# Kernel optimization log

Hardware: AMD Instinct MI355X
Metric: run time of the kernel (lower is better)

Reference implementation:

```python
import jax, jax.numpy as jnp
import numpy as np

HEADS = 8
IN_C = 256
MDL = 512
N = 4
L = 4096
NE = 65536  # avg degree 16


def setup_inputs() -> dict:
    key = jax.random.key(0)
    ks = jax.random.split(key, 14)
    f32 = jnp.float32
    s = 0.05
    return {
        "queries": jax.random.normal(ks[0], (N, L, IN_C), f32),
        "keys": jax.random.normal(ks[1], (N, L, IN_C), f32),
        "values": jax.random.normal(ks[2], (N, L, IN_C), f32),
        "adj": jax.random.randint(ks[3], (2, NE), 0, L, dtype=jnp.int32),
        "edge_pos_enc": jax.random.normal(ks[4], (N, HEADS, NE), f32),
        "Wq": jax.random.normal(ks[5], (IN_C, MDL), f32) * s,
        "bq": jnp.zeros((MDL,), f32),
        "Wk": jax.random.normal(ks[6], (IN_C, MDL), f32) * s,
        "bk": jnp.zeros((MDL,), f32),
        "Wv": jax.random.normal(ks[7], (IN_C, MDL), f32) * s,
        "bv": jnp.zeros((MDL,), f32),
        "Wo": jax.random.normal(ks[8], (MDL, MDL), f32) * s,
        "bo": jnp.zeros((MDL,), f32),
    }


def reference(queries, keys, values, adj, edge_pos_enc, Wq, bq, Wk, bk, Wv, bv, Wo, bo):
    n, l, _ = queries.shape
    h = HEADS
    e = MDL // h  # per-head dim
    temp = 1.0 / jnp.sqrt(jnp.asarray(e, queries.dtype))
    dst, src = adj[0], adj[1]

    def split(x):  # (n, l, mdl) -> (n*h, l, e)
        return x.reshape(n, l, h, e).transpose(0, 2, 1, 3).reshape(n * h, l, e)

    q = split(queries @ Wq + bq)
    k = split(keys @ Wk + bk)
    v = split(values @ Wv + bv)
    epe = edge_pos_enc.reshape(n * h, NE)

    def head(qh, kh, vh, eh):
        # qh,kh,vh: (l, e); eh: (Ne,)
        scores = temp * (jnp.sum(qh[dst] * kh[src], axis=-1) + eh)  # (Ne,)
        m = jax.ops.segment_max(scores, dst, num_segments=l)
        p = jnp.exp(scores - m[dst])
        z = jax.ops.segment_sum(p, dst, num_segments=l)
        alpha = p / z[dst]  # segment softmax keyed by dst (adj[0])
        return jax.ops.segment_sum(alpha[:, None] * vh[src], dst, num_segments=l)  # (l, e)

    out = jax.vmap(head)(q, k, v, epe)  # (n*h, l, e)
    out = out.reshape(n, h, l, e).transpose(0, 2, 1, 3).reshape(n, l, h * e)
    return out @ Wo + bo
```

## Files before the change

### kernel.cpp

```cpp
#include <hip/hip_runtime.h>
#include <hip/hip_bf16.h>
#include <math.h>
#include <stdint.h>

#define HEADS 8
#define IN_C  256
#define MDL   512
#define NB    4
#define LL    4096
#define NE    65536
#define EDIM  64
#define TEMP  0.125f

typedef __bf16 bf16x8 __attribute__((ext_vector_type(8)));
typedef float  f32x4  __attribute__((ext_vector_type(4)));
typedef short  short8 __attribute__((ext_vector_type(8)));

__device__ __forceinline__ void glds16(const void* g, void* l) {
    __builtin_amdgcn_global_load_lds(
        (const __attribute__((address_space(1))) void*)g,
        (__attribute__((address_space(3))) void*)l, 16, 0, 0);
}

__device__ __forceinline__ bf16x8 cvt8b(float4 a, float4 b) {
    union { short8 s; bf16x8 v; __hip_bfloat16 h[8]; } u;
    u.h[0] = __float2bfloat16(a.x); u.h[1] = __float2bfloat16(a.y);
    u.h[2] = __float2bfloat16(a.z); u.h[3] = __float2bfloat16(a.w);
    u.h[4] = __float2bfloat16(b.x); u.h[5] = __float2bfloat16(b.y);
    u.h[6] = __float2bfloat16(b.z); u.h[7] = __float2bfloat16(b.w);
    return u.v;
}

__global__ __launch_bounds__(256) void gemm_qkv(
    const float* __restrict__ A0, const float* __restrict__ A1,
    const float* __restrict__ A2,
    const __hip_bfloat16* __restrict__ B0, const __hip_bfloat16* __restrict__ B1,
    const __hip_bfloat16* __restrict__ B2,
    const float* __restrict__ b0, const float* __restrict__ b1,
    const float* __restrict__ b2,
    __hip_bfloat16* __restrict__ C0, __hip_bfloat16* __restrict__ C1,
    __hip_bfloat16* __restrict__ C2)
{
    __shared__ __align__(16) float          Asf[2 * 128 * 32];
    __shared__ __align__(16) __hip_bfloat16 Bsh[2 * 128 * 32];

    const int K = IN_C, N = MDL;
    const int lin  = blockIdx.x;
    const int xcd  = lin & 7;
    const int t0   = lin >> 3;
    const int z    = t0 >> 6;
    const int rest = t0 & 63;
    const int bm   = (xcd * 16 + (rest & 15)) * 128;
    const int bn   = (rest >> 4) * 128;

    const float* A           = (z == 0) ? A0 : (z == 1) ? A1 : A2;
    const __hip_bfloat16* Bt = (z == 0) ? B0 : (z == 1) ? B1 : B2;
    const float* bias        = (z == 0) ? b0 : (z == 1) ? b1 : b2;
    __hip_bfloat16* C        = (z == 0) ? C0 : (z == 1) ? C1 : C2;

    const int tid  = threadIdx.x;
    const int lane = tid & 63;
    const int w    = tid >> 6;
    const int wr   = w >> 1, wc = w & 1;

    const float* gAc[4]; float* lAc[4];
    #pragma unroll
    for (int i = 0; i < 4; i++) {
        int idx  = i * 256 + tid;
        int rr   = idx >> 3;
        int cpos = idx & 7;
        int cdat = cpos ^ (rr & 7);
        gAc[i] = A + (size_t)(bm + rr) * K + cdat * 4;
        lAc[i] = Asf + rr * 32 + cpos * 4;
    }
    const __hip_bfloat16* gBc[2]; __hip_bfloat16* lBc[2];
    #pragma unroll
    for (int i = 0; i < 2; i++) {
        int idx  = i * 256 + tid;
        int rr   = idx >> 2;
        int cpos = idx & 3;
        int cdat = cpos ^ ((rr >> 1) & 3);
        gBc[i] = Bt + (size_t)(bn + rr) * K + cdat * 8;
        lBc[i] = Bsh + rr * 32 + cpos * 8;
    }

    int rA[4], rB[4];
    #pragma unroll
    for (int i = 0; i < 4; i++) {
        rA[i] = wr * 64 + i * 16 + (lane & 15);
        rB[i] = wc * 64 + i * 16 + (lane & 15);
    }
    const int cq = lane >> 4;

    #define STAGE_QKV(kk, buf) do {                                        \
        _Pragma("unroll")                                                  \
        for (int i = 0; i < 4; i++)                                        \
            glds16(gAc[i] + (kk) * 32, lAc[i] + (buf) * 4096);             \
        _Pragma("unroll")                                                  \
        for (int i = 0; i < 2; i++)                                        \
            glds16(gBc[i] + (kk) * 32, lBc[i] + (buf) * 4096);             \
    } while (0)

    f32x4 acc[4][4] = {};

    STAGE_QKV(0, 0);
    STAGE_QKV(1, 1);

    #pragma unroll
    for (int t = 0; t < 8; ++t) {
        if (t < 7) asm volatile("s_waitcnt vmcnt(6)" ::: "memory");
        else       asm volatile("s_waitcnt vmcnt(0)" ::: "memory");
        __builtin_amdgcn_sched_barrier(0);
        __builtin_amdgcn_s_barrier();
        __builtin_amdgcn_sched_barrier(0);

        const int buf = t & 1;
        const float*          Ab = Asf + buf * 4096;
        const __hip_bfloat16* Bb = Bsh + buf * 4096;

        bf16x8 am[4], bv[4];
        #pragma unroll
        for (int mi = 0; mi < 4; mi++) {
            int c0 = cq * 2;
            int p0 = c0 ^ (rA[mi] & 7);
            int p1 = (c0 + 1) ^ (rA[mi] & 7);
            float4 x = *(const float4*)(Ab + rA[mi] * 32 + p0 * 4);
            float4 y = *(const float4*)(Ab + rA[mi] * 32 + p1 * 4);
            am[mi] = cvt8b(x, y);
        }
        #pragma unroll
        for (int ni = 0; ni < 4; ni++) {
            int p = cq ^ ((rB[ni] >> 1) & 3);
            bv[ni] = *(const bf16x8*)(Bb + rB[ni] * 32 + p * 8);
        }
        #pragma unroll
        for (int mi = 0; mi < 4; mi++)
            #pragma unroll
            for (int ni = 0; ni < 4; ni++)
                acc[mi][ni] = __builtin_amdgcn_mfma_f32_16x16x32_bf16(
                    am[mi], bv[ni], acc[mi][ni], 0, 0, 0);

        asm volatile("" ::: "memory");
        __builtin_amdgcn_sched_barrier(0);
        __builtin_amdgcn_s_barrier();
        if (t < 6) STAGE_QKV(t + 2, buf);
    }
    #undef STAGE_QKV

    #pragma unroll
    for (int mi = 0; mi < 4; mi++) {
        int row = bm + wr * 64 + mi * 16 + (lane >> 4) * 4;
        #pragma unroll
        for (int ni = 0; ni < 4; ni++) {
            int col = bn + wc * 64 + ni * 16 + (lane & 15);
            float bb = bias[col];
            #pragma unroll
            for (int j = 0; j < 4; j++)
                C[(size_t)(row + j) * N + col] = __float2bfloat16(acc[mi][ni][j] + bb);
        }
    }
}

__global__ __launch_bounds__(256) void gemm_out(
    const __hip_bfloat16* __restrict__ A, const __hip_bfloat16* __restrict__ Bt,
    const float* __restrict__ bias, float* __restrict__ C)
{
    __shared__ __align__(16) __hip_bfloat16 Asb[2 * 128 * 32];
    __shared__ __align__(16) __hip_bfloat16 Bsb[2 * 64 * 32];

    const int K = MDL, N = MDL;
    const int lin = blockIdx.x;
    const int xcd = lin & 7;
    const int t0  = lin >> 3;
    const int bm  = (xcd * 16 + (t0 & 15)) * 128;
    const int bn  = (t0 >> 4) * 64;

    const int tid  = threadIdx.x;
    const int lane = tid & 63;
    const int w    = tid >> 6;

    const __hip_bfloat16* gAc[2]; __hip_bfloat16* lAc[2];
    #pragma unroll
    for (int i = 0; i < 2; i++) {
        int idx  = i * 256 + tid;
        int rr   = idx >> 2;
        int cpos = idx & 3;
        int cdat = cpos ^ ((rr >> 1) & 3);
        gAc[i] = A + (size_t)(bm + rr) * K + cdat * 8;
        lAc[i] = Asb + rr * 32 + cpos * 8;
    }
    const __hip_bfloat16* gBc; __hip_bfloat16* lBc;
    {
        int rr   = tid >> 2;
        int cpos = tid & 3;
        int cdat = cpos ^ ((rr >> 1) & 3);
        gBc = Bt + (size_t)(bn + rr) * K + cdat * 8;
        lBc = Bsb + rr * 32 + cpos * 8;
    }

    int rA[2], rB[4];
    #pragma unroll
    for (int i = 0; i < 2; i++) rA[i] = w * 32 + i * 16 + (lane & 15);
    #pragma unroll
    for (int i = 0; i < 4; i++) rB[i] = i * 16 + (lane & 15);
    const int cq = lane >> 4;

    #define STAGE_OUT(kk, buf) do {                                        \
        _Pragma("unroll")                                                  \
        for (int i = 0; i < 2; i++)                                        \
            glds16(gAc[i] + (kk) * 32, lAc[i] + (buf) * 4096);             \
        glds16(gBc + (kk) * 32, lBc + (buf) * 2048);                       \
    } while (0)

    f32x4 acc[2][4] = {};

    STAGE_OUT(0, 0);
    STAGE_OUT(1, 1);

    #pragma unroll
    for (int t = 0; t < 16; ++t) {
        if (t < 15) asm volatile("s_waitcnt vmcnt(3)" ::: "memory");
        else        asm volatile("s_waitcnt vmcnt(0)" ::: "memory");
        __builtin_amdgcn_sched_barrier(0);
        __builtin_amdgcn_s_barrier();
        __builtin_amdgcn_sched_barrier(0);

        const int buf = t & 1;
        const __hip_bfloat16* Ab = Asb + buf * 4096;
        const __hip_bfloat16* Bb = Bsb + buf * 2048;

        bf16x8 am[2], bv[4];
        #pragma unroll
        for (int mi = 0; mi < 2; mi++) {
            int p = cq ^ ((rA[mi] >> 1) & 3);
            am[mi] = *(const bf16x8*)(Ab + rA[mi] * 32 + p * 8);
        }
        #pragma unroll
        for (int ni = 0; ni < 4; ni++) {
            int p = cq ^ ((rB[ni] >> 1) & 3);
            bv[ni] = *(const bf16x8*)(Bb + rB[ni] * 32 + p * 8);
        }
        #pragma unroll
        for (int mi = 0; mi < 2; mi++)
            #pragma unroll
            for (int ni = 0; ni < 4; ni++)
                acc[mi][ni] = __builtin_amdgcn_mfma_f32_16x16x32_bf16(
                    am[mi], bv[ni], acc[mi][ni], 0, 0, 0);

        asm volatile("" ::: "memory");
        __builtin_amdgcn_sched_barrier(0);
        __builtin_amdgcn_s_barrier();
        if (t < 14) STAGE_OUT(t + 2, buf);
    }
    #undef STAGE_OUT

    #pragma unroll
    for (int mi = 0; mi < 2; mi++) {
        int row = bm + w * 32 + mi * 16 + (lane >> 4) * 4;
        #pragma unroll
        for (int ni = 0; ni < 4; ni++) {
            int col = bn + ni * 16 + (lane & 15);
            float bb = bias[col];
            #pragma unroll
            for (int j = 0; j < 4; j++)
                C[(size_t)(row + j) * N + col] = acc[mi][ni][j] + bb;
        }
    }
}

__global__ __launch_bounds__(1024) void csr_build(
    const int* __restrict__ dst, int* __restrict__ offsets,
    int* __restrict__ cursor, int* __restrict__ reorder)
{
    __shared__ int hist[4096];
    __shared__ int wsum[16];
    __shared__ int bcnt[9], boff[9];
    const int tid  = threadIdx.x;
    const int lane = tid & 63;
    const int wid  = tid >> 6;

    #pragma unroll
    for (int i = 0; i < 4; i++) hist[tid + i * 1024] = 0;
    if (tid < 9) bcnt[tid] = 0;
    __syncthreads();

    const int4* d4 = (const int4*)dst;
    #pragma unroll
    for (int i = 0; i < 16; i++) {
        int4 v = d4[i * 1024 + tid];
        atomicAdd(&hist[v.x], 1);
        atomicAdd(&hist[v.y], 1);
        atomicAdd(&hist[v.z], 1);
        atomicAdd(&hist[v.w], 1);
    }
    __syncthreads();

    int c[4];
    int base = tid * 4;
    int s = 0;
    #pragma unroll
    for (int i = 0; i < 4; i++) { c[i] = hist[base + i]; s += c[i]; }

    int v = s;
    #pragma unroll
    for (int off = 1; off < 64; off <<= 1) {
        int t = __shfl_up(v, off);
        if (lane >= off) v += t;
    }
    if (lane == 63) wsum[wid] = v;
    __syncthreads();
    if (wid == 0) {
        int wv = (lane < 16) ? wsum[lane] : 0;
        #pragma unroll
        for (int off = 1; off < 16; off <<= 1) {
            int t = __shfl_up(wv, off);
            if (lane >= off) wv += t;
        }
        if (lane < 16) wsum[lane] = wv;
    }
    __syncthreads();

    int prefix = (wid > 0 ? wsum[wid - 1] : 0) + (v - s);
    int run = prefix;
    int mybk[4];
    #pragma unroll
    for (int i = 0; i < 4; i++) {
        offsets[base + i] = run;
        cursor[base + i]  = run;
        run += c[i];
        int sc = (c[i] + 7) >> 3; if (sc > 8) sc = 8;
        mybk[i] = 8 - sc;
        atomicAdd(&bcnt[mybk[i]], 1);
    }
    if (tid == 1023) offsets[4096] = run;
    __syncthreads();
    if (tid == 0) {
        int acc0 = 0;
        #pragma unroll
        for (int b = 0; b < 9; b++) { boff[b] = acc0; acc0 += bcnt[b]; }
    }
    __syncthreads();
    #pragma unroll
    for (int i = 0; i < 4; i++) {
        int pos = atomicAdd(&boff[mybk[i]], 1);
        reorder[pos] = base + i;
    }
}

__global__ __launch_bounds__(256) void prep(
    const int* __restrict__ dst, const int* __restrict__ srcarr,
    const float* __restrict__ epe, int* __restrict__ cursor,
    int* __restrict__ src_s, float* __restrict__ epe_s,
    const float* __restrict__ Wq, const float* __restrict__ Wk,
    const float* __restrict__ Wv, const float* __restrict__ Wo,
    __hip_bfloat16* __restrict__ Wqt, __hip_bfloat16* __restrict__ Wkt,
    __hip_bfloat16* __restrict__ Wvt, __hip_bfloat16* __restrict__ Wot)
{
    __shared__ float t[32][33];
    const int b = blockIdx.x;

    if (b < 256) {
        int e = b * 256 + threadIdx.x;
        int p = atomicAdd(&cursor[dst[e]], 1);
        src_s[p] = srcarr[e];
        #pragma unroll
        for (int n = 0; n < NB; n++) {
            float4 a2, b2;
            const float* base = epe + (size_t)(n * HEADS) * NE + e;
            a2.x = base[0 * NE]; a2.y = base[1 * NE]; a2.z = base[2 * NE]; a2.w = base[3 * NE];
            b2.x = base[4 * NE]; b2.y = base[5 * NE]; b2.z = base[6 * NE]; b2.w = base[7 * NE];
            float* o = epe_s + ((size_t)n * NE + p) * 8;
            *(float4*)o       = a2;
            *(float4*)(o + 4) = b2;
        }
    } else {
        int bb = b - 256;
        const float* W; __hip_bfloat16* Wt; int K, tt;
        if (bb < 384) {
            int m = bb >> 7; tt = bb & 127; K = IN_C;
            W  = (m == 0) ? Wq  : (m == 1) ? Wk  : Wv;
            Wt = (m == 0) ? Wqt : (m == 1) ? Wkt : Wvt;
        } else {
            tt = bb - 384; K = MDL; W = Wo; Wt = Wot;
        }
        const int N = MDL;
        int bx = (tt & 15) * 32;
        int by = (tt >> 4) * 32;
        int tx = threadIdx.x & 31, ty = threadIdx.x >> 5;
        #pragma unroll
        for (int i = 0; i < 4; i++)
            t[ty + i * 8][tx] = W[(size_t)(by + ty + i * 8) * N + bx + tx];
        __syncthreads();
        #pragma unroll
        for (int i = 0; i < 4; i++)
            Wt[(size_t)(bx + ty + i * 8) * K + by + tx] =
                __float2bfloat16(t[tx][ty + i * 8]);
    }
}

__global__ __launch_bounds__(256) void sparse_score(
    const __hip_bfloat16* __restrict__ Qb, const __hip_bfloat16* __restrict__ Kb,
    const int* __restrict__ src_s, const float* __restrict__ epe_s,
    const int* __restrict__ offsets, const int* __restrict__ reorder,
    float* __restrict__ score_s, float2* __restrict__ mz)
{
    const int lane = threadIdx.x & 63;
    const int wid  = threadIdx.x >> 6;
    const int bid  = blockIdx.x;
    const int xcd  = bid & 7;
    const int n    = xcd >> 1;
    const int base = ((bid >> 3) << 1) | (xcd & 1);
    const int dstn = reorder[(base << 2) | wid];
    const int task = n * LL + dstn;
    const int hg   = lane >> 3;

    const int beg = offsets[dstn];
    const int end = offsets[dstn + 1];
    const int deg = end - beg;
    if (deg == 0) return;

    bf16x8 q8 = *(const bf16x8*)(Qb + (size_t)task * MDL + lane * 8);
    float qf[8];
    #pragma unroll
    for (int j = 0; j < 8; j++) qf[j] = (float)q8[j];

    const __hip_bfloat16* Kn = Kb + (size_t)n * LL * MDL + lane * 8;
    const float* pe_n = epe_s + (size_t)n * NE * 8 + hg;
    float* sc_n = score_s + (size_t)n * NE * 8 + hg;

    float m = -INFINITY, z = 0.0f;

    if (deg <= 64) {
        const int my_src = src_s[beg + ((lane < deg) ? lane : (deg - 1))];

        #pragma unroll
        for (int slot = 0; slot < 8; slot++) {
            const int r0 = slot * 8;
            if (r0 < deg) {
                bf16x8 kk[8];
                #pragma unroll
                for (int j = 0; j < 8; j++) {
                    int s = __shfl(my_src, r0 + j);
                    kk[j] = *(const bf16x8*)(Kn + (size_t)s * MDL);
                }
                const int rel_mine = r0 + (lane & 7);
                float pp = (rel_mine < deg)
                         ? pe_n[(size_t)(beg + rel_mine) * 8] : -INFINITY;

                float p[8];
                #pragma unroll
                for (int j = 0; j < 8; j++) {
                    float d = 0.0f;
                    #pragma unroll
                    for (int dd = 0; dd < 8; dd++)
                        d = fmaf(qf[dd], (float)kk[j][dd], d);
                    p[j] = d;
                }
                float n0, n1, n2, n3, u0, u1, sraw;
                {
                    float a0 = (lane & 1) ? p[1] : p[0];
                    float b0 = (lane & 1) ? p[0] : p[1];
                    n0 = a0 + __shfl_xor(b0, 1);
                    float a1 = (lane & 1) ? p[3] : p[2];
                    float b1 = (lane & 1) ? p[2] : p[3];
                    n1 = a1 + __shfl_xor(b1, 1);
                    float a2 = (lane & 1) ? p[5] : p[4];
                    float b2 = (lane & 1) ? p[4] : p[5];
                    n2 = a2 + __shfl_xor(b2, 1);
                    float a3 = (lane & 1) ? p[7] : p[6];
                    float b3 = (lane & 1) ? p[6] : p[7];
                    n3 = a3 + __shfl_xor(b3, 1);

                    float c0 = (lane & 2) ? n1 : n0;
                    float d0 = (lane & 2) ? n0 : n1;
                    u0 = c0 + __shfl_xor(d0, 2);
                    float c1 = (lane & 2) ? n3 : n2;
                    float d1 = (lane & 2) ? n2 : n3;
                    u1 = c1 + __shfl_xor(d1, 2);

                    float e0 = (lane & 4) ? u1 : u0;
                    float f0 = (lane & 4) ? u0 : u1;
                    sraw = e0 + __shfl_xor(f0, 4);
                }

                float sc_my = TEMP * (sraw + pp);
                if (rel_mine < deg)
                    sc_n[(size_t)(beg + rel_mine) * 8] = sc_my;

                float gm = sc_my;
                gm = fmaxf(gm, __shfl_xor(gm, 1));
                gm = fmaxf(gm, __shfl_xor(gm, 2));
                gm = fmaxf(gm, __shfl_xor(gm, 4));
                float mnew = fmaxf(m, gm);
                float e_my = __expf(sc_my - mnew);
                float gs = e_my;
                gs += __shfl_xor(gs, 1);
                gs += __shfl_xor(gs, 2);
                gs += __shfl_xor(gs, 4);
                z = z * __expf(m - mnew) + gs;
                m = mnew;
            }
        }
    } else {
        for (int i = beg; i < end; i += 4) {
            float sc4[4];
            #pragma unroll
            for (int j = 0; j < 4; j++) {
                int idx = i + j;
                int ok  = idx < end;
                int s   = ok ? src_s[idx] : src_s[beg];
                bf16x8 kk = *(const bf16x8*)(Kn + (size_t)s * MDL);
                float pp = ok ? pe_n[(size_t)idx * 8] : -INFINITY;
                float d = 0.0f;
                #pragma unroll
                for (int dd = 0; dd < 8; dd++) d += qf[dd] * (float)kk[dd];
                d += __shfl_xor(d, 1);
                d += __shfl_xor(d, 2);
                d += __shfl_xor(d, 4);
                sc4[j] = TEMP * (d + pp);
                if (ok && (lane & 7) == 0)
                    sc_n[(size_t)idx * 8] = sc4[j];
            }
            float mb   = fmaxf(fmaxf(sc4[0], sc4[1]), fmaxf(sc4[2], sc4[3]));
            float mnew = fmaxf(m, mb);
            float sc   = __expf(m - mnew);
            float s0 = __expf(sc4[0] - mnew);
            float s1 = __expf(sc4[1] - mnew);
            float s2 = __expf(sc4[2] - mnew);
            float s3 = __expf(sc4[3] - mnew);
            z = z * sc + (s0 + s1 + s2 + s3);
            m = mnew;
        }
    }

    if ((lane & 7) == 0) {
        float2 v; v.x = m; v.y = 1.0f / z;
        mz[(size_t)task * 8 + hg] = v;
    }
}

__global__ __launch_bounds__(256) void sparse_out(
    const __hip_bfloat16* __restrict__ Vb,
    const int* __restrict__ src_s, const float* __restrict__ score_s,
    const int* __restrict__ offsets, const int* __restrict__ reorder,
    const float2* __restrict__ mz, __hip_bfloat16* __restrict__ O)
{
    const int lane = threadIdx.x & 63;
    const int wid  = threadIdx.x >> 6;
    const int bid  = blockIdx.x;
    const int xcd  = bid & 7;
    const int n    = xcd >> 1;
    const int base = ((bid >> 3) << 1) | (xcd & 1);
    const int dstn = reorder[(base << 2) | wid];
    const int task = n * LL + dstn;
    const int hg   = lane >> 3;

    const size_t rowbase = (size_t)task * MDL;
    const int beg = offsets[dstn];
    const int end = offsets[dstn + 1];
    const int deg = end - beg;

    union { short8 v8; __hip_bfloat16 h[8]; } uo;
    if (deg == 0) {
        #pragma unroll
        for (int j = 0; j < 8; j++) uo.h[j] = __float2bfloat16(0.0f);
        *(short8*)(O + rowbase + lane * 8) = uo.v8;
        return;
    }

    float2 mzv = mz[(size_t)task * 8 + hg];
    const float m = mzv.x, zinv = mzv.y;

    const __hip_bfloat16* Vn = Vb + (size_t)n * LL * MDL + lane * 8;
    const float* sc_n = score_s + (size_t)n * NE * 8 + hg;

    float acc[8] = {};

    if (deg <= 64) {
        const int my_src = src_s[beg + ((lane < deg) ? lane : (deg - 1))];

        #pragma unroll
        for (int slot = 0; slot < 8; slot++) {
            const int r0 = slot * 8;
            if (r0 < deg) {
                bf16x8 vv[8];
                #pragma unroll
                for (int j = 0; j < 8; j++) {
                    int s = __shfl(my_src, r0 + j);
                    vv[j] = *(const bf16x8*)(Vn + (size_t)s * MDL);
                }
                const int rel_mine = r0 + (lane & 7);
                float sc = (rel_mine < deg)
                         ? sc_n[(size_t)(beg + rel_mine) * 8] : -INFINITY;
                float a_l = __expf(sc - m) * zinv;
                #pragma unroll
                for (int j = 0; j < 8; j++) {
                    float al = __shfl(a_l, (lane & 56) | j);
                    #pragma unroll
                    for (int dd = 0; dd < 8; dd++)
                        acc[dd] = fmaf(al, (float)vv[j][dd], acc[dd]);
                }
            }
        }
    } else {
        for (int i = beg; i < end; i += 4) {
            #pragma unroll
            for (int j = 0; j < 4; j++) {
                int idx = i + j;
                int ok  = idx < end;
                int s   = ok ? src_s[idx] : src_s[beg];
                bf16x8 vv = *(const bf16x8*)(Vn + (size_t)s * MDL);
                float sc = ok ? sc_n[(size_t)idx * 8] : -INFINITY;
                float al = __expf(sc - m) * zinv;
                #pragma unroll
                for (int dd = 0; dd < 8; dd++)
                    acc[dd] = fmaf(al, (float)vv[dd], acc[dd]);
            }
        }
    }

    #pragma unroll
    for (int j = 0; j < 8; j++) uo.h[j] = __float2bfloat16(acc[j]);
    *(short8*)(O + rowbase + lane * 8) = uo.v8;
}

extern "C" void kernel_launch(void* const* d_in, const int* in_sizes, int n_in,
                              void* d_out, int out_size, void* d_ws, size_t ws_size,
                              hipStream_t stream)
{
    const float* queries = (const float*)d_in[0];
    const float* keys    = (const float*)d_in[1];
    const float* values  = (const float*)d_in[2];
    const int*   adj     = (const int*)d_in[3];
    const float* epe     = (const float*)d_in[4];
    const float* Wq = (const float*)d_in[5];
    const float* bq = (const float*)d_in[6];
    const float* Wk = (const float*)d_in[7];
    const float* bk = (const float*)d_in[8];
    const float* Wv = (const float*)d_in[9];
    const float* bv = (const float*)d_in[10];
    const float* Wo = (const float*)d_in[11];
    const float* bo = (const float*)d_in[12];
    float* out = (float*)d_out;

    const int* dst = adj;
    const int* src = adj + NE;

    const int    M   = NB * LL;
    const size_t NLM = (size_t)M * MDL;

    char* w = (char*)d_ws;
    __hip_bfloat16* Qb  = (__hip_bfloat16*)w; w += NLM * 2;
    __hip_bfloat16* Kb  = (__hip_bfloat16*)w; w += NLM * 2;
    __hip_bfloat16* Vb  = (__hip_bfloat16*)w; w += NLM * 2;
    __hip_bfloat16* Ob  = (__hip_bfloat16*)w; w += NLM * 2;
    __hip_bfloat16* Wqt = (__hip_bfloat16*)w; w += (size_t)MDL * IN_C * 2;
    __hip_bfloat16* Wkt = (__hip_bfloat16*)w; w += (size_t)MDL * IN_C * 2;
    __hip_bfloat16* Wvt = (__hip_bfloat16*)w; w += (size_t)MDL * IN_C * 2;
    __hip_bfloat16* Wot = (__hip_bfloat16*)w; w += (size_t)MDL * MDL * 2;
    int* offsets = (int*)w; w += 4100 * sizeof(int);
    int* cursor  = (int*)w; w += 4096 * sizeof(int);
    int* reorder = (int*)w; w += 4096 * sizeof(int);
    int*   src_s = (int*)w; w += NE * sizeof(int);
    float* epe_s   = (float*)w;  w += (size_t)NB * NE * 8 * sizeof(float);
    float* score_s = (float*)w;  w += (size_t)NB * NE * 8 * sizeof(float);
    float2* mz     = (float2*)w; w += (size_t)M * 8 * sizeof(float2);

    csr_build<<<1, 1024, 0, stream>>>(dst, offsets, cursor, reorder);

    prep<<<896, 256, 0, stream>>>(dst, src, epe, cursor, src_s, epe_s,
                                  Wq, Wk, Wv, Wo, Wqt, Wkt, Wvt, Wot);

    gemm_qkv<<<1536, 256, 0, stream>>>(queries, keys, values, Wqt, Wkt, Wvt,
                                       bq, bk, bv, Qb, Kb, Vb);

    sparse_score<<<(NB * LL) / 4, 256, 0, stream>>>(Qb, Kb, src_s, epe_s,
                                                    offsets, reorder, score_s, mz);
    sparse_out<<<(NB * LL) / 4, 256, 0, stream>>>(Vb, src_s, score_s,
                                                  offsets, reorder, mz, Ob);

    gemm_out<<<1024, 256, 0, stream>>>(Ob, Wot, bo, out);
}
```

Before: 119.2 us.

## Drop double buffering in GEMMs for occupancy and shrink output GEMM tile

```diff
diff --git a/kernel.cpp b/kernel.cpp
--- a/kernel.cpp
+++ b/kernel.cpp
@@ -31,7 +31,7 @@
     return u.v;
 }
 
-__global__ __launch_bounds__(256) void gemm_qkv(
+__global__ __launch_bounds__(256, 6) void gemm_qkv(
     const float* __restrict__ A0, const float* __restrict__ A1,
     const float* __restrict__ A2,
     const __hip_bfloat16* __restrict__ B0, const __hip_bfloat16* __restrict__ B1,
@@ -41,8 +41,8 @@
     __hip_bfloat16* __restrict__ C0, __hip_bfloat16* __restrict__ C1,
     __hip_bfloat16* __restrict__ C2)
 {
-    __shared__ __align__(16) float          Asf[2 * 128 * 32];
-    __shared__ __align__(16) __hip_bfloat16 Bsh[2 * 128 * 32];
+    __shared__ __align__(16) float          Asf[128 * 32];
+    __shared__ __align__(16) __hip_bfloat16 Bsh[128 * 32];
 
     const int K = IN_C, N = MDL;
     const int lin  = blockIdx.x;
@@ -92,31 +92,14 @@
     }
     const int cq = lane >> 4;
 
-    #define STAGE_QKV(kk, buf) do {                                        \
-        _Pragma("unroll")                                                  \
-        for (int i = 0; i < 4; i++)                                        \
-            glds16(gAc[i] + (kk) * 32, lAc[i] + (buf) * 4096);             \
-        _Pragma("unroll")                                                  \
-        for (int i = 0; i < 2; i++)                                        \
-            glds16(gBc[i] + (kk) * 32, lBc[i] + (buf) * 4096);             \
-    } while (0)
-
     f32x4 acc[4][4] = {};
 
-    STAGE_QKV(0, 0);
-    STAGE_QKV(1, 1);
-
-    #pragma unroll
     for (int t = 0; t < 8; ++t) {
-        if (t < 7) asm volatile("s_waitcnt vmcnt(6)" ::: "memory");
-        else       asm volatile("s_waitcnt vmcnt(0)" ::: "memory");
-        __builtin_amdgcn_sched_barrier(0);
-        __builtin_amdgcn_s_barrier();
-        __builtin_amdgcn_sched_barrier(0);
-
-        const int buf = t & 1;
-        const float*          Ab = Asf + buf * 4096;
-        const __hip_bfloat16* Bb = Bsh + buf * 4096;
+        #pragma unroll
+        for (int i = 0; i < 4; i++) glds16(gAc[i] + t * 32, lAc[i]);
+        #pragma unroll
+        for (int i = 0; i < 2; i++) glds16(gBc[i] + t * 32, lBc[i]);
+        __syncthreads();
 
         bf16x8 am[4], bv[4];
         #pragma unroll
@@ -124,14 +107,14 @@
             int c0 = cq * 2;
             int p0 = c0 ^ (rA[mi] & 7);
             int p1 = (c0 + 1) ^ (rA[mi] & 7);
-            float4 x = *(const float4*)(Ab + rA[mi] * 32 + p0 * 4);
-            float4 y = *(const float4*)(Ab + rA[mi] * 32 + p1 * 4);
+            float4 x = *(const float4*)(Asf + rA[mi] * 32 + p0 * 4);
+            float4 y = *(const float4*)(Asf + rA[mi] * 32 + p1 * 4);
             am[mi] = cvt8b(x, y);
         }
         #pragma unroll
         for (int ni = 0; ni < 4; ni++) {
             int p = cq ^ ((rB[ni] >> 1) & 3);
-            bv[ni] = *(const bf16x8*)(Bb + rB[ni] * 32 + p * 8);
+            bv[ni] = *(const bf16x8*)(Bsh + rB[ni] * 32 + p * 8);
         }
         #pragma unroll
         for (int mi = 0; mi < 4; mi++)
@@ -139,13 +122,8 @@
             for (int ni = 0; ni < 4; ni++)
                 acc[mi][ni] = __builtin_amdgcn_mfma_f32_16x16x32_bf16(
                     am[mi], bv[ni], acc[mi][ni], 0, 0, 0);
-
-        asm volatile("" ::: "memory");
-        __builtin_amdgcn_sched_barrier(0);
-        __builtin_amdgcn_s_barrier();
-        if (t < 6) STAGE_QKV(t + 2, buf);
-    }
-    #undef STAGE_QKV
+        __syncthreads();
+    }
 
     #pragma unroll
     for (int mi = 0; mi < 4; mi++) {
@@ -161,33 +139,31 @@
     }
 }
 
-__global__ __launch_bounds__(256) void gemm_out(
+__global__ __launch_bounds__(256, 8) void gemm_out(
     const __hip_bfloat16* __restrict__ A, const __hip_bfloat16* __restrict__ Bt,
     const float* __restrict__ bias, float* __restrict__ C)
 {
-    __shared__ __align__(16) __hip_bfloat16 Asb[2 * 128 * 32];
-    __shared__ __align__(16) __hip_bfloat16 Bsb[2 * 64 * 32];
+    __shared__ __align__(16) __hip_bfloat16 Asb[64 * 32];
+    __shared__ __align__(16) __hip_bfloat16 Bsb[64 * 32];
 
     const int K = MDL, N = MDL;
     const int lin = blockIdx.x;
     const int xcd = lin & 7;
     const int t0  = lin >> 3;
-    const int bm  = (xcd * 16 + (t0 & 15)) * 128;
-    const int bn  = (t0 >> 4) * 64;
+    const int bm  = (xcd * 32 + (t0 & 31)) * 64;
+    const int bn  = (t0 >> 5) * 64;
 
     const int tid  = threadIdx.x;
     const int lane = tid & 63;
     const int w    = tid >> 6;
 
-    const __hip_bfloat16* gAc[2]; __hip_bfloat16* lAc[2];
-    #pragma unroll
-    for (int i = 0; i < 2; i++) {
-        int idx  = i * 256 + tid;
-        int rr   = idx >> 2;
-        int cpos = idx & 3;
+    const __hip_bfloat16* gAc; __hip_bfloat16* lAc;
+    {
+        int rr   = tid >> 2;
+        int cpos = tid & 3;
         int cdat = cpos ^ ((rr >> 1) & 3);
-        gAc[i] = A + (size_t)(bm + rr) * K + cdat * 8;
-        lAc[i] = Asb + rr * 32 + cpos * 8;
+        gAc = A + (size_t)(bm + rr) * K + cdat * 8;
+        lAc = Asb + rr * 32 + cpos * 8;
     }
     const __hip_bfloat16* gBc; __hip_bfloat16* lBc;
     {
@@ -198,72 +174,45 @@
         lBc = Bsb + rr * 32 + cpos * 8;
     }
 
-    int rA[2], rB[4];
-    #pragma unroll
-    for (int i = 0; i < 2; i++) rA[i] = w * 32 + i * 16 + (lane & 15);
+    const int rA = w * 16 + (lane & 15);
+    int rB[4];
     #pragma unroll
     for (int i = 0; i < 4; i++) rB[i] = i * 16 + (lane & 15);
     const int cq = lane >> 4;
 
-    #define STAGE_OUT(kk, buf) do {                                        \
-        _Pragma("unroll")                                                  \
-        for (int i = 0; i < 2; i++)                                        \
-            glds16(gAc[i] + (kk) * 32, lAc[i] + (buf) * 4096);             \
-        glds16(gBc + (kk) * 32, lBc + (buf) * 2048);                       \
-    } while (0)
-
-    f32x4 acc[2][4] = {};
-
-    STAGE_OUT(0, 0);
-    STAGE_OUT(1, 1);
-
-    #pragma unroll
+    f32x4 acc[4] = {};
+
     for (int t = 0; t < 16; ++t) {
-        if (t < 15) asm volatile("s_waitcnt vmcnt(3)" ::: "memory");
-        else        asm volatile("s_waitcnt vmcnt(0)" ::: "memory");
-        __builtin_amdgcn_sched_barrier(0);
-        __builtin_amdgcn_s_barrier();
-        __builtin_amdgcn_sched_barrier(0);
-
-        const int buf = t & 1;
-        const __hip_bfloat16* Ab = Asb + buf * 4096;
-        const __hip_bfloat16* Bb = Bsb + buf * 2048;
-
-        bf16x8 am[2], bv[4];
-        #pragma unroll
-        for (int mi = 0; mi < 2; mi++) {
-            int p = cq ^ ((rA[mi] >> 1) & 3);
-            am[mi] = *(const bf16x8*)(Ab + rA[mi] * 32 + p * 8);
+        glds16(gAc + t * 32, lAc);
+        glds16(gBc + t * 32, lBc);
+        __syncthreads();
+
+        bf16x8 am, bv[4];
+        {
+            int p = cq ^ ((rA >> 1) & 3);
+            am = *(const bf16x8*)(Asb + rA * 32 + p * 8);
         }
         #pragma unroll
         for (int ni = 0; ni < 4; ni++) {
             int p = cq ^ ((rB[ni] >> 1) & 3);
-            bv[ni] = *(const bf16x8*)(Bb + rB[ni] * 32 + p * 8);
-        }
-        #pragma unroll
-        for (int mi = 0; mi < 2; mi++)
-            #pragma unroll
-            for (int ni = 0; ni < 4; ni++)
-                acc[mi][ni] = __builtin_amdgcn_mfma_f32_16x16x32_bf16(
-                    am[mi], bv[ni], acc[mi][ni], 0, 0, 0);
-
-        asm volatile("" ::: "memory");
-        __builtin_amdgcn_sched_barrier(0);
-        __builtin_amdgcn_s_barrier();
-        if (t < 14) STAGE_OUT(t + 2, buf);
-    }
-    #undef STAGE_OUT
-
-    #pragma unroll
-    for (int mi = 0; mi < 2; mi++) {
-        int row = bm + w * 32 + mi * 16 + (lane >> 4) * 4;
+            bv[ni] = *(const bf16x8*)(Bsb + rB[ni] * 32 + p * 8);
+        }
+        #pragma unroll
+        for (int ni = 0; ni < 4; ni++)
+            acc[ni] = __builtin_amdgcn_mfma_f32_16x16x32_bf16(
+                am, bv[ni], acc[ni], 0, 0, 0);
+        __syncthreads();
+    }
+
+    {
+        int row = bm + w * 16 + (lane >> 4) * 4;
         #pragma unroll
         for (int ni = 0; ni < 4; ni++) {
             int col = bn + ni * 16 + (lane & 15);
             float bb = bias[col];
             #pragma unroll
             for (int j = 0; j < 4; j++)
-                C[(size_t)(row + j) * N + col] = acc[mi][ni][j] + bb;
+                C[(size_t)(row + j) * N + col] = acc[ni][j] + bb;
         }
     }
 }
@@ -679,5 +628,5 @@
     sparse_out<<<(NB * LL) / 4, 256, 0, stream>>>(Vb, src_s, score_s,
                                                   offsets, reorder, mz, Ob);
 
-    gemm_out<<<1024, 256, 0, stream>>>(Ob, Wot, bo, out);
-}
+    gemm_out<<<2048, 256, 0, stream>>>(Ob, Wot, bo, out);
+}
```

Result: slower. 252.6 us (+111.9%).
